# Performance work log

Measured on AMD Instinct MI355X. Metric: run time of the kernel, lower is better.

## Reference

```python
import jax, jax.numpy as jnp
import numpy as np

BETA = 0.95
THR = 1.0
NUM_STEPS = 100
ALPHA = 2.0  # snntorch atan surrogate default

@jax.custom_vjp
def atan_spike(x):
    return (x > 0).astype(x.dtype)

def _as_fwd(x):
    return (x > 0).astype(x.dtype), x

def _as_bwd(x, g):
    return (g * (ALPHA / 2) / (1 + (jnp.pi / 2 * ALPHA * x) ** 2),)

atan_spike.defvjp(_as_fwd, _as_bwd)


def setup_inputs() -> dict:
    key = jax.random.key(0)
    ks = jax.random.split(key, 9)
    B = 16384
    SH, NH, CO, OUT = 1024, 1024, 256, 64
    s = 0.05
    return {
        "x": jax.random.normal(ks[0], (B, 105), jnp.float32),
        "snn_w1": jax.random.normal(ks[1], (SH, 5), jnp.float32) * s,
        "snn_b1": jnp.zeros((SH,), jnp.float32),
        "snn_w2": jax.random.normal(ks[2], (OUT, SH), jnp.float32) * s,
        "snn_b2": jnp.zeros((OUT,), jnp.float32),
        "nn_w1": jax.random.normal(ks[3], (NH, 5), jnp.float32) * s,
        "nn_b1": jnp.zeros((NH,), jnp.float32),
        "nn_w2": jax.random.normal(ks[4], (OUT, NH), jnp.float32) * s,
        "nn_b2": jnp.zeros((OUT,), jnp.float32),
        "conv_w": jax.random.normal(ks[5], (32, 1, 3), jnp.float32) * s,
        "conv_b": jnp.zeros((32,), jnp.float32),
        "cnn_fc_w": jax.random.normal(ks[6], (CO, 32 * 50), jnp.float32) * s,
        "cnn_fc_b": jnp.zeros((CO,), jnp.float32),
        "comb_w": jax.random.normal(ks[7], (OUT, 2 * OUT + CO), jnp.float32) * s,
        "comb_b": jnp.zeros((OUT,), jnp.float32),
    }


def _forward(x, snn_w1, snn_b1, snn_w2, snn_b2, nn_w1, nn_b1, nn_w2, nn_b2,
             conv_w, conv_b, cnn_fc_w, cnn_fc_b, comb_w, comb_b):
    feats = x[:, :5]                 # [B,5]
    wave = x[:, 5:][:, None, :]      # [B,1,100]
    B = x.shape[0]

    # ---- SNN branch (LIF, beta leak, subtract reset, threshold 1.0) ----
    cur1 = feats @ snn_w1.T + snn_b1  # input current is constant across steps

    def step(carry, _):
        mem1, spk1, mem2, spk2 = carry
        # reset term uses detached spike (snntorch mem_reset detaches)
        mem1 = BETA * mem1 + cur1 - jax.lax.stop_gradient(spk1) * THR
        spk1 = atan_spike(mem1 - THR)
        cur2 = spk1 @ snn_w2.T + snn_b2
        mem2 = BETA * mem2 + cur2 - jax.lax.stop_gradient(spk2) * THR
        spk2 = atan_spike(mem2 - THR)
        return (mem1, spk1, mem2, spk2), spk2

    z1 = jnp.zeros_like(cur1)
    z2 = jnp.zeros((B, snn_w2.shape[0]), cur1.dtype)
    _, spk_rec = jax.lax.scan(step, (z1, z1, z2, z2), None, length=NUM_STEPS)
    snn_out = spk_rec.mean(axis=0)   # [B,OUT]

    # ---- MLP branch ----
    nn_out = jax.nn.relu(feats @ nn_w1.T + nn_b1) @ nn_w2.T + nn_b2

    # ---- CNN branch ----
    c = jax.lax.conv_general_dilated(wave, conv_w, (1,), [(1, 1)],
                                     dimension_numbers=("NCW", "OIW", "NCW"))
    c = jax.nn.relu(c + conv_b[None, :, None])   # [B,32,100]
    c = c.reshape(B, 32, 50, 2).max(axis=-1)      # MaxPool1d(k=2,s=2)
    cnn_out = c.reshape(B, -1) @ cnn_fc_w.T + cnn_fc_b

    combined = jnp.concatenate([snn_out, nn_out, cnn_out], axis=1)
    return combined @ comb_w.T + comb_b


def reference(x, snn_w1, snn_b1, snn_w2, snn_b2, nn_w1, nn_b1, nn_w2, nn_b2,
              conv_w, conv_b, cnn_fc_w, cnn_fc_b, comb_w, comb_b):
    return _forward(x, snn_w1, snn_b1, snn_w2, snn_b2, nn_w1, nn_b1, nn_w2,
                    nn_b2, conv_w, conv_b, cnn_fc_w, cnn_fc_b, comb_w, comb_b)
```

## Files before the change

### kernel.cpp

```cpp
#include <hip/hip_runtime.h>

typedef __bf16 bf16x8_t __attribute__((ext_vector_type(8)));
typedef float f32x4_t __attribute__((ext_vector_type(4)));

#define NSTEPS 100
#define PB0 0u
#define PB1 32768u
#define COMBF 51200u

static __device__ __forceinline__ unsigned short f2bfu(float v) {
  union { __bf16 h; unsigned short u; } c; c.h = (__bf16)v; return c.u;
}
static __device__ __forceinline__ unsigned int pack2bf(float a, float b) {
  return (unsigned)f2bfu(a) | ((unsigned)f2bfu(b) << 16);
}
union BF8U { unsigned int u[4]; bf16x8_t v; };

static __device__ __forceinline__ bf16x8_t bfrag_f32(const float* __restrict__ p, float s) {
  BF8U r;
#pragma unroll
  for (int i = 0; i < 4; ++i) r.u[i] = pack2bf(p[2*i]*s, p[2*i+1]*s);
  return r.v;
}

static __device__ __forceinline__ void comb_store(unsigned char* ldsp, int k, int row, float v) {
  *(unsigned short*)(ldsp + COMBF +
      (unsigned)((k >> 5)*1024 + (((k >> 3) & 3)*16 + row)*16 + (k & 7)*2)) = f2bfu(v);
}

__global__ __launch_bounds__(512, 2)
void hybrid_v4(const float* __restrict__ x,
               const float* __restrict__ snn_w1, const float* __restrict__ snn_b1,
               const float* __restrict__ snn_w2, const float* __restrict__ snn_b2,
               const float* __restrict__ nn_w1,  const float* __restrict__ nn_b1,
               const float* __restrict__ nn_w2,  const float* __restrict__ nn_b2,
               const float* __restrict__ conv_w, const float* __restrict__ conv_b,
               const float* __restrict__ fc_w,   const float* __restrict__ fc_b,
               const float* __restrict__ comb_w, const float* __restrict__ comb_b,
               const unsigned short* __restrict__ fcwb, int use_bf,
               float* __restrict__ out)
{
  __shared__ __align__(16) unsigned char lds[65536];
  const int tid  = threadIdx.x;
  const int w    = tid >> 6;
  const int l    = tid & 63;
  const int q    = l >> 4;
  const int m    = l & 15;
  const int row0 = blockIdx.x * 16;

  const int hi  = w >> 2;
  const int ntr = w & 3;
  const int rn  = ntr*16 + m;
  const int rA  = hi*4 + q;
  const int rB  = rA + 8;

  const float* xr = x + (row0 + m)*105;
  const float f0 = xr[0], f1 = xr[1], f2 = xr[2], f3 = xr[3], f4 = xr[4];
  const float b2l = snn_b2[rn];

  bf16x8_t bfr[4][4];
#pragma unroll
  for (int ci = 0; ci < 4; ++ci)
#pragma unroll
    for (int nt = 0; nt < 4; ++nt)
      bfr[ci][nt] = bfrag_f32(snn_w2 + (nt*16 + m)*1024 + (w*4 + ci)*32 + q*8, 1.f);

  float c[32], mem[32];
  {
    const int kb = w*128 + q*8;
#pragma unroll
    for (int ci = 0; ci < 4; ++ci) {
      const float* wp = snn_w1 + (kb + ci*32)*5;
      float wa[40];
#pragma unroll
      for (int u2 = 0; u2 < 10; ++u2) {
        const float4 t4 = *(const float4*)(wp + u2*4);
        wa[u2*4+0] = t4.x; wa[u2*4+1] = t4.y; wa[u2*4+2] = t4.z; wa[u2*4+3] = t4.w;
      }
#pragma unroll
      for (int j = 0; j < 8; ++j) {
        c[ci*8+j] = f0*wa[j*5] + f1*wa[j*5+1] + f2*wa[j*5+2] + f3*wa[j*5+3] + f4*wa[j*5+4]
                  + snn_b1[kb + ci*32 + j];
        mem[ci*8+j] = 0.f;
      }
    }
  }

  BF8U afr[4];
  auto lif_update_pack = [&]() {
#pragma unroll
    for (int i = 0; i < 32; ++i) {
      const float sp = mem[i] > 1.f ? 1.f : 0.f;
      mem[i] = __fsub_rn(__fadd_rn(__fmul_rn(0.95f, mem[i]), c[i]), sp);
    }
#pragma unroll
    for (int ci = 0; ci < 4; ++ci)
#pragma unroll
      for (int jj = 0; jj < 4; ++jj)
        afr[ci].u[jj] = (mem[ci*8 + 2*jj]   > 1.f ? 0x3F80u     : 0u)
                      | (mem[ci*8 + 2*jj+1] > 1.f ? 0x3F800000u : 0u);
  };
  lif_update_pack();

  float m2A = 0.f, s2A = 0.f, cntA = 0.f;
  float m2B = 0.f, s2B = 0.f, cntB = 0.f;

  const unsigned pbase  = (unsigned)(ntr*1024 + hi*256 + m*16 + q*4);
  const unsigned wtbase = (unsigned)((w*4*64 + l)*16);
  const f32x4_t z4 = {0.f, 0.f, 0.f, 0.f};

  auto phase = [&](unsigned cur, unsigned prv, bool doRead, bool doLif) {
    float vA[8], vB[8];
    if (doRead) {
#pragma unroll
      for (int s = 0; s < 8; ++s) vA[s] = *(const float*)(lds + prv + pbase + (unsigned)(s*4096));
#pragma unroll
      for (int s = 0; s < 8; ++s) vB[s] = *(const float*)(lds + prv + pbase + 512u + (unsigned)(s*4096));
    }
    f32x4_t acc[4] = {z4, z4, z4, z4};
#pragma unroll
    for (int ci = 0; ci < 4; ++ci)
#pragma unroll
      for (int nt = 0; nt < 4; ++nt)
        acc[nt] = __builtin_amdgcn_mfma_f32_16x16x32_bf16(afr[ci].v, bfr[ci][nt], acc[nt], 0,0,0);
#pragma unroll
    for (int nt = 0; nt < 4; ++nt)
      *(f32x4_t*)(lds + cur + wtbase + (unsigned)(nt*1024)) = acc[nt];
    if (doLif) lif_update_pack();
    if (doRead) {
      float curA = (((vA[0]+vA[1]) + (vA[2]+vA[3])) + ((vA[4]+vA[5]) + (vA[6]+vA[7]))) + b2l;
      float curB = (((vB[0]+vB[1]) + (vB[2]+vB[3])) + ((vB[4]+vB[5]) + (vB[6]+vB[7]))) + b2l;
      m2A = __fsub_rn(__fadd_rn(__fmul_rn(0.95f, m2A), curA), s2A);
      s2A = m2A > 1.f ? 1.f : 0.f;  cntA += s2A;
      m2B = __fsub_rn(__fadd_rn(__fmul_rn(0.95f, m2B), curB), s2B);
      s2B = m2B > 1.f ? 1.f : 0.f;  cntB += s2B;
    }
    __syncthreads();
  };

#pragma unroll 1
  for (int tt = 0; tt < NSTEPS; tt += 2) {
    phase(PB0, PB1, tt > 0, true);
    phase(PB1, PB0, true,  tt + 1 < NSTEPS - 1);
  }

#pragma unroll
  for (int ci = 0; ci < 4; ++ci)
#pragma unroll
    for (int nt = 0; nt < 4; ++nt)
      bfr[ci][nt] = bfrag_f32(nn_w2 + (nt*16 + m)*1024 + (w*4 + ci)*32 + q*8, 1.f);
  {
    float vA[8], vB[8];
#pragma unroll
    for (int s = 0; s < 8; ++s) vA[s] = *(const float*)(lds + PB1 + pbase + (unsigned)(s*4096));
#pragma unroll
    for (int s = 0; s < 8; ++s) vB[s] = *(const float*)(lds + PB1 + pbase + 512u + (unsigned)(s*4096));
    float curA = (((vA[0]+vA[1]) + (vA[2]+vA[3])) + ((vA[4]+vA[5]) + (vA[6]+vA[7]))) + b2l;
    float curB = (((vB[0]+vB[1]) + (vB[2]+vB[3])) + ((vB[4]+vB[5]) + (vB[6]+vB[7]))) + b2l;
    m2A = __fsub_rn(__fadd_rn(__fmul_rn(0.95f, m2A), curA), s2A);
    s2A = m2A > 1.f ? 1.f : 0.f;  cntA += s2A;
    m2B = __fsub_rn(__fadd_rn(__fmul_rn(0.95f, m2B), curB), s2B);
    s2B = m2B > 1.f ? 1.f : 0.f;  cntB += s2B;

    BF8U hfr[4];
    const int kb = w*128 + q*8;
#pragma unroll
    for (int ci = 0; ci < 4; ++ci) {
      const float* wp = nn_w1 + (kb + ci*32)*5;
      float wa[40];
#pragma unroll
      for (int u2 = 0; u2 < 10; ++u2) {
        const float4 t4 = *(const float4*)(wp + u2*4);
        wa[u2*4+0] = t4.x; wa[u2*4+1] = t4.y; wa[u2*4+2] = t4.z; wa[u2*4+3] = t4.w;
      }
      float hv[8];
#pragma unroll
      for (int j = 0; j < 8; ++j) {
        const float h = f0*wa[j*5] + f1*wa[j*5+1] + f2*wa[j*5+2] + f3*wa[j*5+3] + f4*wa[j*5+4]
                      + nn_b1[kb + ci*32 + j];
        hv[j] = fmaxf(h, 0.f);
      }
#pragma unroll
      for (int jj = 0; jj < 4; ++jj) hfr[ci].u[jj] = pack2bf(hv[2*jj], hv[2*jj+1]);
    }
    f32x4_t acc[4] = {z4, z4, z4, z4};
#pragma unroll
    for (int ci = 0; ci < 4; ++ci)
#pragma unroll
      for (int nt = 0; nt < 4; ++nt)
        acc[nt] = __builtin_amdgcn_mfma_f32_16x16x32_bf16(hfr[ci].v, bfr[ci][nt], acc[nt], 0,0,0);
#pragma unroll
    for (int nt = 0; nt < 4; ++nt)
      *(f32x4_t*)(lds + PB0 + wtbase + (unsigned)(nt*1024)) = acc[nt];
  }
  __syncthreads();
  {
    float vA[8], vB[8];
#pragma unroll
    for (int s = 0; s < 8; ++s) vA[s] = *(const float*)(lds + PB0 + pbase + (unsigned)(s*4096));
#pragma unroll
    for (int s = 0; s < 8; ++s) vB[s] = *(const float*)(lds + PB0 + pbase + 512u + (unsigned)(s*4096));
    const float nA = (((vA[0]+vA[1]) + (vA[2]+vA[3])) + ((vA[4]+vA[5]) + (vA[6]+vA[7]))) + nn_b2[rn];
    const float nB = (((vB[0]+vB[1]) + (vB[2]+vB[3])) + ((vB[4]+vB[5]) + (vB[6]+vB[7]))) + nn_b2[rn];
    comb_store(lds, rn,      rA, cntA * 0.0078125f);
    comb_store(lds, rn,      rB, cntB * 0.0078125f);
    comb_store(lds, 64 + rn, rA, nA);
    comb_store(lds, 64 + rn, rB, nB);
  }
  __syncthreads();

  {
    const int ch = tid >> 4;
    const float cw0 = conv_w[ch*3+0], cw1 = conv_w[ch*3+1], cw2 = conv_w[ch*3+2];
    const float cbb = conv_b[ch];
    const float* xw = xr + 5;
    float xm1 = 0.f, x0v = xw[0];
#pragma unroll 1
    for (int p = 0; p < 50; ++p) {
      const float xp1 = xw[2*p + 1];
      const float xp2 = (p < 49) ? xw[2*p + 2] : 0.f;
      const float av = cw0*xm1 + cw1*x0v + cw2*xp1 + cbb;
      const float bv = cw0*x0v + cw1*xp1 + cw2*xp2 + cbb;
      const float pv = fmaxf(fmaxf(av, 0.f), fmaxf(bv, 0.f));
      const int k = ch*50 + p;
      *(unsigned short*)(lds + (unsigned)((k>>5)*1024 + (((k>>3)&3)*16 + m)*16 + (k&7)*2)) = f2bfu(pv);
      xm1 = xp1; x0v = xp2;
    }
  }
  __syncthreads();

  {
    const int c0 = (w*2 + 0)*16 + m;
    const int c1 = (w*2 + 1)*16 + m;
    f32x4_t e0 = z4, o0 = z4, e1 = z4, o1 = z4;
    if (use_bf) {
#pragma unroll 2
      for (int kc = 0; kc < 50; kc += 2) {
        const bf16x8_t a0 = *(const bf16x8_t*)(lds + (unsigned)((kc*64 + l)*16));
        const bf16x8_t a1 = *(const bf16x8_t*)(lds + (unsigned)(((kc+1)*64 + l)*16));
        e0 = __builtin_amdgcn_mfma_f32_16x16x32_bf16(a0, *(const bf16x8_t*)(fcwb + c0*1600 + kc*32 + q*8), e0, 0,0,0);
        o0 = __builtin_amdgcn_mfma_f32_16x16x32_bf16(a1, *(const bf16x8_t*)(fcwb + c0*1600 + (kc+1)*32 + q*8), o0, 0,0,0);
        e1 = __builtin_amdgcn_mfma_f32_16x16x32_bf16(a0, *(const bf16x8_t*)(fcwb + c1*1600 + kc*32 + q*8), e1, 0,0,0);
        o1 = __builtin_amdgcn_mfma_f32_16x16x32_bf16(a1, *(const bf16x8_t*)(fcwb + c1*1600 + (kc+1)*32 + q*8), o1, 0,0,0);
      }
    } else {
#pragma unroll 2
      for (int kc = 0; kc < 50; kc += 2) {
        const bf16x8_t a0 = *(const bf16x8_t*)(lds + (unsigned)((kc*64 + l)*16));
        const bf16x8_t a1 = *(const bf16x8_t*)(lds + (unsigned)(((kc+1)*64 + l)*16));
        e0 = __builtin_amdgcn_mfma_f32_16x16x32_bf16(a0, bfrag_f32(fc_w + c0*1600 + kc*32 + q*8, 1.f), e0, 0,0,0);
        o0 = __builtin_amdgcn_mfma_f32_16x16x32_bf16(a1, bfrag_f32(fc_w + c0*1600 + (kc+1)*32 + q*8, 1.f), o0, 0,0,0);
        e1 = __builtin_amdgcn_mfma_f32_16x16x32_bf16(a0, bfrag_f32(fc_w + c1*1600 + kc*32 + q*8, 1.f), e1, 0,0,0);
        o1 = __builtin_amdgcn_mfma_f32_16x16x32_bf16(a1, bfrag_f32(fc_w + c1*1600 + (kc+1)*32 + q*8, 1.f), o1, 0,0,0);
      }
    }
    const float fb0 = fc_b[c0], fb1 = fc_b[c1];
#pragma unroll
    for (int r = 0; r < 4; ++r) {
      comb_store(lds, 128 + c0, q*4 + r, (e0[r] + o0[r]) + fb0);
      comb_store(lds, 128 + c1, q*4 + r, (e1[r] + o1[r]) + fb1);
    }
  }
  __syncthreads();

  if (w < 4) {
    const int cn = w*16 + m;
    f32x4_t oe = z4, oo = z4;
#pragma unroll
    for (int kc = 0; kc < 12; kc += 2) {
      const bf16x8_t a0 = *(const bf16x8_t*)(lds + COMBF + (unsigned)((kc*64 + l)*16));
      const bf16x8_t a1 = *(const bf16x8_t*)(lds + COMBF + (unsigned)(((kc+1)*64 + l)*16));
      const float s0 = (kc    < 2) ? 1.28f : 1.f;
      const float s1 = (kc+1 < 2) ? 1.28f : 1.f;
      oe = __builtin_amdgcn_mfma_f32_16x16x32_bf16(a0, bfrag_f32(comb_w + cn*384 + kc*32 + q*8, s0), oe, 0,0,0);
      oo = __builtin_amdgcn_mfma_f32_16x16x32_bf16(a1, bfrag_f32(comb_w + cn*384 + (kc+1)*32 + q*8, s1), oo, 0,0,0);
    }
    const float cb2 = comb_b[cn];
#pragma unroll
    for (int r = 0; r < 4; ++r)
      out[(row0 + q*4 + r)*64 + cn] = (oe[r] + oo[r]) + cb2;
  }
}

__global__ __launch_bounds__(256)
void fcw_to_bf16(const float* __restrict__ src, unsigned short* __restrict__ dst) {
  const int i = (blockIdx.x * 256 + threadIdx.x) * 4;
  const float4 v = *(const float4*)(src + i);
  ushort4 o;
  o.x = f2bfu(v.x); o.y = f2bfu(v.y); o.z = f2bfu(v.z); o.w = f2bfu(v.w);
  *(ushort4*)(dst + i) = o;
}

extern "C" void kernel_launch(void* const* d_in, const int* in_sizes, int n_in,
                              void* d_out, int out_size, void* d_ws, size_t ws_size,
                              hipStream_t stream) {
  const float* x       = (const float*)d_in[0];
  const float* snn_w1  = (const float*)d_in[1];
  const float* snn_b1  = (const float*)d_in[2];
  const float* snn_w2  = (const float*)d_in[3];
  const float* snn_b2  = (const float*)d_in[4];
  const float* nn_w1   = (const float*)d_in[5];
  const float* nn_b1   = (const float*)d_in[6];
  const float* nn_w2   = (const float*)d_in[7];
  const float* nn_b2   = (const float*)d_in[8];
  const float* conv_w  = (const float*)d_in[9];
  const float* conv_b  = (const float*)d_in[10];
  const float* fc_w    = (const float*)d_in[11];
  const float* fc_b    = (const float*)d_in[12];
  const float* comb_w  = (const float*)d_in[13];
  const float* comb_b  = (const float*)d_in[14];
  float* outp = (float*)d_out;

  const int rows = in_sizes[0] / 105;
  const int grid = rows / 16;

  const size_t fcw_elems = (size_t)in_sizes[11];
  const int use_bf = (ws_size >= fcw_elems * 2) ? 1 : 0;
  unsigned short* fcwb = (unsigned short*)d_ws;
  if (use_bf) {
    fcw_to_bf16<<<dim3((unsigned)(fcw_elems / 1024)), dim3(256), 0, stream>>>(fc_w, fcwb);
  }

  hybrid_v4<<<dim3(grid), dim3(512), 0, stream>>>(
      x, snn_w1, snn_b1, snn_w2, snn_b2,
      nn_w1, nn_b1, nn_w2, nn_b2,
      conv_w, conv_b, fc_w, fc_b, comb_w, comb_b,
      fcwb, use_bf, outp);
}
```

Before: 722.1 us.

## Quadruple-buffer SNN partial sums in LDS to halve barriers per step

The SNN time loop now handles two timesteps per iteration using four 32KB partial-sum buffers in dynamic LDS, so only one __syncthreads is needed per two steps instead of one per step. This is meant to cut barrier stalls and let MFMA work for one step overlap with the reduction reads of the previous pair. The cost is doubling LDS to 128KB per block, raised through hipFuncSetAttribute. That likely allows only one 512-thread block per CU instead of two, reducing occupancy and latency hiding.

```diff
diff --git a/kernel.cpp b/kernel.cpp
--- a/kernel.cpp
+++ b/kernel.cpp
@@ -4,9 +4,11 @@
 typedef float f32x4_t __attribute__((ext_vector_type(4)));
 
 #define NSTEPS 100
-#define PB0 0u
-#define PB1 32768u
-#define COMBF 51200u
+#define PART0 0u
+#define PART1 32768u
+#define PART2 65536u
+#define PART3 98304u
+#define COMBF 118784u
 
 static __device__ __forceinline__ unsigned short f2bfu(float v) {
   union { __bf16 h; unsigned short u; } c; c.h = (__bf16)v; return c.u;
@@ -29,7 +31,7 @@
 }
 
 __global__ __launch_bounds__(512, 2)
-void hybrid_v4(const float* __restrict__ x,
+void hybrid_v6(const float* __restrict__ x,
                const float* __restrict__ snn_w1, const float* __restrict__ snn_b1,
                const float* __restrict__ snn_w2, const float* __restrict__ snn_b2,
                const float* __restrict__ nn_w1,  const float* __restrict__ nn_b1,
@@ -40,7 +42,7 @@
                const unsigned short* __restrict__ fcwb, int use_bf,
                float* __restrict__ out)
 {
-  __shared__ __align__(16) unsigned char lds[65536];
+  extern __shared__ __align__(16) unsigned char lds[];
   const int tid  = threadIdx.x;
   const int w    = tid >> 6;
   const int l    = tid & 63;
@@ -109,14 +111,7 @@
   const unsigned wtbase = (unsigned)((w*4*64 + l)*16);
   const f32x4_t z4 = {0.f, 0.f, 0.f, 0.f};
 
-  auto phase = [&](unsigned cur, unsigned prv, bool doRead, bool doLif) {
-    float vA[8], vB[8];
-    if (doRead) {
-#pragma unroll
-      for (int s = 0; s < 8; ++s) vA[s] = *(const float*)(lds + prv + pbase + (unsigned)(s*4096));
-#pragma unroll
-      for (int s = 0; s < 8; ++s) vB[s] = *(const float*)(lds + prv + pbase + 512u + (unsigned)(s*4096));
-    }
+  auto do_mfma_store = [&](unsigned cur) {
     f32x4_t acc[4] = {z4, z4, z4, z4};
 #pragma unroll
     for (int ci = 0; ci < 4; ++ci)
@@ -126,8 +121,24 @@
 #pragma unroll
     for (int nt = 0; nt < 4; ++nt)
       *(f32x4_t*)(lds + cur + wtbase + (unsigned)(nt*1024)) = acc[nt];
-    if (doLif) lif_update_pack();
-    if (doRead) {
+  };
+
+#pragma unroll 1
+  for (int p = 0; p < NSTEPS/2; ++p) {
+    const unsigned cur0 = (p & 1) ? PART2 : PART0;
+    const unsigned cur1 = cur0 + 32768u;
+    const unsigned prv0 = (p & 1) ? PART0 : PART2;
+    const unsigned prv1 = prv0 + 32768u;
+
+    float vA[8], vB[8];
+    if (p > 0) {
+#pragma unroll
+      for (int s = 0; s < 8; ++s) vA[s] = *(const float*)(lds + prv0 + pbase + (unsigned)(s*4096));
+#pragma unroll
+      for (int s = 0; s < 8; ++s) vB[s] = *(const float*)(lds + prv0 + pbase + 512u + (unsigned)(s*4096));
+    }
+    do_mfma_store(cur0);
+    if (p > 0) {
       float curA = (((vA[0]+vA[1]) + (vA[2]+vA[3])) + ((vA[4]+vA[5]) + (vA[6]+vA[7]))) + b2l;
       float curB = (((vB[0]+vB[1]) + (vB[2]+vB[3])) + ((vB[4]+vB[5]) + (vB[6]+vB[7]))) + b2l;
       m2A = __fsub_rn(__fadd_rn(__fmul_rn(0.95f, m2A), curA), s2A);
@@ -135,13 +146,25 @@
       m2B = __fsub_rn(__fadd_rn(__fmul_rn(0.95f, m2B), curB), s2B);
       s2B = m2B > 1.f ? 1.f : 0.f;  cntB += s2B;
     }
+    float uA[8], uB[8];
+    if (p > 0) {
+#pragma unroll
+      for (int s = 0; s < 8; ++s) uA[s] = *(const float*)(lds + prv1 + pbase + (unsigned)(s*4096));
+#pragma unroll
+      for (int s = 0; s < 8; ++s) uB[s] = *(const float*)(lds + prv1 + pbase + 512u + (unsigned)(s*4096));
+    }
+    lif_update_pack();
+    do_mfma_store(cur1);
+    if (p > 0) {
+      float curA = (((uA[0]+uA[1]) + (uA[2]+uA[3])) + ((uA[4]+uA[5]) + (uA[6]+uA[7]))) + b2l;
+      float curB = (((uB[0]+uB[1]) + (uB[2]+uB[3])) + ((uB[4]+uB[5]) + (uB[6]+uB[7]))) + b2l;
+      m2A = __fsub_rn(__fadd_rn(__fmul_rn(0.95f, m2A), curA), s2A);
+      s2A = m2A > 1.f ? 1.f : 0.f;  cntA += s2A;
+      m2B = __fsub_rn(__fadd_rn(__fmul_rn(0.95f, m2B), curB), s2B);
+      s2B = m2B > 1.f ? 1.f : 0.f;  cntB += s2B;
+    }
+    if (p < NSTEPS/2 - 1) lif_update_pack();
     __syncthreads();
-  };
-
-#pragma unroll 1
-  for (int tt = 0; tt < NSTEPS; tt += 2) {
-    phase(PB0, PB1, tt > 0, true);
-    phase(PB1, PB0, true,  tt + 1 < NSTEPS - 1);
   }
 
 #pragma unroll
@@ -152,15 +175,25 @@
   {
     float vA[8], vB[8];
 #pragma unroll
-    for (int s = 0; s < 8; ++s) vA[s] = *(const float*)(lds + PB1 + pbase + (unsigned)(s*4096));
-#pragma unroll
-    for (int s = 0; s < 8; ++s) vB[s] = *(const float*)(lds + PB1 + pbase + 512u + (unsigned)(s*4096));
+    for (int s = 0; s < 8; ++s) vA[s] = *(const float*)(lds + PART2 + pbase + (unsigned)(s*4096));
+#pragma unroll
+    for (int s = 0; s < 8; ++s) vB[s] = *(const float*)(lds + PART2 + pbase + 512u + (unsigned)(s*4096));
     float curA = (((vA[0]+vA[1]) + (vA[2]+vA[3])) + ((vA[4]+vA[5]) + (vA[6]+vA[7]))) + b2l;
     float curB = (((vB[0]+vB[1]) + (vB[2]+vB[3])) + ((vB[4]+vB[5]) + (vB[6]+vB[7]))) + b2l;
     m2A = __fsub_rn(__fadd_rn(__fmul_rn(0.95f, m2A), curA), s2A);
     s2A = m2A > 1.f ? 1.f : 0.f;  cntA += s2A;
     m2B = __fsub_rn(__fadd_rn(__fmul_rn(0.95f, m2B), curB), s2B);
     s2B = m2B > 1.f ? 1.f : 0.f;  cntB += s2B;
+#pragma unroll
+    for (int s = 0; s < 8; ++s) vA[s] = *(const float*)(lds + PART3 + pbase + (unsigned)(s*4096));
+#pragma unroll
+    for (int s = 0; s < 8; ++s) vB[s] = *(const float*)(lds + PART3 + pbase + 512u + (unsigned)(s*4096));
+    curA = (((vA[0]+vA[1]) + (vA[2]+vA[3])) + ((vA[4]+vA[5]) + (vA[6]+vA[7]))) + b2l;
+    curB = (((vB[0]+vB[1]) + (vB[2]+vB[3])) + ((vB[4]+vB[5]) + (vB[6]+vB[7]))) + b2l;
+    m2A = __fsub_rn(__fadd_rn(__fmul_rn(0.95f, m2A), curA), s2A);
+    s2A = m2A > 1.f ? 1.f : 0.f;  cntA += s2A;
+    m2B = __fsub_rn(__fadd_rn(__fmul_rn(0.95f, m2B), curB), s2B);
+    s2B = m2B > 1.f ? 1.f : 0.f;  cntB += s2B;
 
     BF8U hfr[4];
     const int kb = w*128 + q*8;
@@ -191,15 +224,15 @@
         acc[nt] = __builtin_amdgcn_mfma_f32_16x16x32_bf16(hfr[ci].v, bfr[ci][nt], acc[nt], 0,0,0);
 #pragma unroll
     for (int nt = 0; nt < 4; ++nt)
-      *(f32x4_t*)(lds + PB0 + wtbase + (unsigned)(nt*1024)) = acc[nt];
+      *(f32x4_t*)(lds + PART0 + wtbase + (unsigned)(nt*1024)) = acc[nt];
   }
   __syncthreads();
   {
     float vA[8], vB[8];
 #pragma unroll
-    for (int s = 0; s < 8; ++s) vA[s] = *(const float*)(lds + PB0 + pbase + (unsigned)(s*4096));
-#pragma unroll
-    for (int s = 0; s < 8; ++s) vB[s] = *(const float*)(lds + PB0 + pbase + 512u + (unsigned)(s*4096));
+    for (int s = 0; s < 8; ++s) vA[s] = *(const float*)(lds + PART0 + pbase + (unsigned)(s*4096));
+#pragma unroll
+    for (int s = 0; s < 8; ++s) vB[s] = *(const float*)(lds + PART0 + pbase + 512u + (unsigned)(s*4096));
     const float nA = (((vA[0]+vA[1]) + (vA[2]+vA[3])) + ((vA[4]+vA[5]) + (vA[6]+vA[7]))) + nn_b2[rn];
     const float nB = (((vB[0]+vB[1]) + (vB[2]+vB[3])) + ((vB[4]+vB[5]) + (vB[6]+vB[7]))) + nn_b2[rn];
     comb_store(lds, rn,      rA, cntA * 0.0078125f);
@@ -314,6 +347,9 @@
   const int rows = in_sizes[0] / 105;
   const int grid = rows / 16;
 
+  (void)hipFuncSetAttribute((const void*)hybrid_v6,
+                            hipFuncAttributeMaxDynamicSharedMemorySize, 131072);
+
   const size_t fcw_elems = (size_t)in_sizes[11];
   const int use_bf = (ws_size >= fcw_elems * 2) ? 1 : 0;
   unsigned short* fcwb = (unsigned short*)d_ws;
@@ -321,7 +357,7 @@
     fcw_to_bf16<<<dim3((unsigned)(fcw_elems / 1024)), dim3(256), 0, stream>>>(fc_w, fcwb);
   }
 
-  hybrid_v4<<<dim3(grid), dim3(512), 0, stream>>>(
+  hybrid_v6<<<dim3(grid), dim3(512), 131072, stream>>>(
       x, snn_w1, snn_b1, snn_w2, snn_b2,
       nn_w1, nn_b1, nn_w2, nn_b2,
       conv_w, conv_b, fc_w, fc_b, comb_w, comb_b,
```

New measurement: 805.1 us. +11.5%, slower.
